# Optimization experiments

Hardware: AMD Instinct MI355X
Metric: run time of the kernel (lower is better)

## Reference

```python
import jax, jax.numpy as jnp
import numpy as np

N = 100000
E = 1600000
D_IN = 128
H = 128


def _param(key, shape, scale=0.05):
    return jax.random.normal(key, shape, dtype=jnp.float32) * scale


def setup_inputs() -> dict:
    key = jax.random.key(0)
    ks = jax.random.split(key, 24)
    inp = {
        'x': jax.random.normal(ks[0], (N, D_IN), dtype=jnp.float32),
        'edge_index': jax.random.randint(ks[1], (2, E), 0, N, dtype=jnp.int64),
        'h1': jax.random.normal(ks[2], (N, H), dtype=jnp.float32),
        'h2': jax.random.normal(ks[3], (N, H), dtype=jnp.float32),
        'h3': jax.random.normal(ks[4], (N, H), dtype=jnp.float32),
        # GCNConv params (PyG: lin weight applied as x @ W, W: [in, out] here)
        'gcn1_w': _param(ks[5], (D_IN, H)),
        'gcn1_b': jnp.zeros((H,), jnp.float32),
        'gcn2_w': _param(ks[6], (H, H)),
        'gcn2_b': jnp.zeros((H,), jnp.float32),
    }
    # torch.nn.GRUCell params: weight_ih [3H, in], weight_hh [3H, H], biases [3H]
    for i, kw in zip((1, 2, 3), (ks[7], ks[10], ks[13])):
        k1, k2, k3 = jax.random.split(kw, 3)
        inp[f'gru{i}_wih'] = _param(k1, (3 * H, H))
        inp[f'gru{i}_whh'] = _param(k2, (3 * H, H))
        inp[f'gru{i}_bih'] = _param(k3, (3 * H,))
        inp[f'gru{i}_bhh'] = jnp.zeros((3 * H,), jnp.float32)
    return inp


def gcn_conv(x, src, dst, w, b):
    """PyG GCNConv: D^-1/2 (A+I) D^-1/2 X W + b (symmetric norm, self-loops)."""
    xw = x @ w  # [N, H]
    ones = jnp.ones((src.shape[0],), xw.dtype)
    # degree including self-loop
    deg = jax.ops.segment_sum(ones, dst, num_segments=N) + 1.0
    dinv = jax.lax.rsqrt(deg)
    norm = dinv[src] * dinv[dst]  # [E]
    agg = jax.ops.segment_sum(xw[src] * norm[:, None], dst, num_segments=N)
    # self-loop contribution: norm = dinv[i]*dinv[i] = 1/deg[i]
    return agg + xw / deg[:, None] + b


def gru_cell(x, h, w_ih, w_hh, b_ih, b_hh):
    gi = x @ w_ih.T + b_ih  # [N, 3H]
    gh = h @ w_hh.T + b_hh
    i_r, i_z, i_n = jnp.split(gi, 3, axis=-1)
    h_r, h_z, h_n = jnp.split(gh, 3, axis=-1)
    r = jax.nn.sigmoid(i_r + h_r)
    z = jax.nn.sigmoid(i_z + h_z)
    n = jnp.tanh(i_n + r * h_n)
    return (1.0 - z) * n + z * h


def reference(x, edge_index, h1, h2, h3,
              gcn1_w, gcn1_b, gcn2_w, gcn2_b,
              gru1_wih, gru1_whh, gru1_bih, gru1_bhh,
              gru2_wih, gru2_whh, gru2_bih, gru2_bhh,
              gru3_wih, gru3_whh, gru3_bih, gru3_bhh):
    src, dst = edge_index[0], edge_index[1]
    x = jax.nn.relu(gcn_conv(x, src, dst, gcn1_w, gcn1_b))
    # dropout is identity at eval
    x = jax.nn.relu(gcn_conv(x, src, dst, gcn2_w, gcn2_b))
    h1n = gru_cell(x, h1, gru1_wih, gru1_whh, gru1_bih, gru1_bhh)
    h2n = gru_cell(h1n, h2, gru2_wih, gru2_whh, gru2_bih, gru2_bhh)
    h3n = gru_cell(h2n, h3, gru3_wih, gru3_whh, gru3_bih, gru3_bhh)
    return (h1n, h2n, h3n)
```

## Files before the change

kernel.cpp:

```cpp
#include <hip/hip_runtime.h>
#include <hip/hip_bf16.h>

#define DH 128
#define SCB 1024
#define NCHUNK 256

typedef __attribute__((ext_vector_type(8))) short short8_t;
typedef __attribute__((ext_vector_type(4))) float f32x4;

static __device__ __forceinline__ short f2bf(float f) {
    union { float f; unsigned u; } v; v.f = f;
    unsigned r = v.u + 0x7fffu + ((v.u >> 16) & 1u);
    return (short)(r >> 16);
}

static __device__ __forceinline__ float bf2f(unsigned short b) {
    union { unsigned u; float f; } v; v.u = ((unsigned)b) << 16;
    return v.f;
}

static __device__ __forceinline__ short8_t cvt8(const float* p) {
    float4 a0 = *(const float4*)p;
    float4 a1 = *(const float4*)(p + 4);
    short8_t t;
    t[0] = f2bf(a0.x); t[1] = f2bf(a0.y); t[2] = f2bf(a0.z); t[3] = f2bf(a0.w);
    t[4] = f2bf(a1.x); t[5] = f2bf(a1.y); t[6] = f2bf(a1.z); t[7] = f2bf(a1.w);
    return t;
}

__global__ __launch_bounds__(256) void deg2_k(const int* __restrict__ ei, int E,
                                              unsigned* __restrict__ cnt, int span, int chunkE) {
    int r = blockIdx.x & 7;
    int c = blockIdx.x >> 3;
    int lo = r * span, hi = lo + span;
    long long e0 = (long long)c * chunkE;
    long long e1 = e0 + chunkE; if (e1 > E) e1 = E;
    for (long long e = e0 + threadIdx.x; e < e1; e += 256) {
        int d = ei[E + e];
        if (d >= lo && d < hi) atomicAdd(&cnt[d], 1u);
    }
}

__global__ __launch_bounds__(256) void scan1_k(const unsigned* __restrict__ cnt, int N,
                                               int* __restrict__ offs, unsigned* __restrict__ bsum) {
    __shared__ unsigned s[256];
    int t = threadIdx.x;
    int i0 = blockIdx.x * SCB + t * 4;
    unsigned v0 = (i0 + 0 < N) ? cnt[i0 + 0] : 0u;
    unsigned v1 = (i0 + 1 < N) ? cnt[i0 + 1] : 0u;
    unsigned v2 = (i0 + 2 < N) ? cnt[i0 + 2] : 0u;
    unsigned v3 = (i0 + 3 < N) ? cnt[i0 + 3] : 0u;
    unsigned ts = v0 + v1 + v2 + v3;
    s[t] = ts;
    __syncthreads();
    for (int off = 1; off < 256; off <<= 1) {
        unsigned u = (t >= off) ? s[t - off] : 0u;
        __syncthreads();
        s[t] += u;
        __syncthreads();
    }
    unsigned ex = s[t] - ts;
    if (i0 + 0 < N) offs[i0 + 0] = (int)ex;
    if (i0 + 1 < N) offs[i0 + 1] = (int)(ex + v0);
    if (i0 + 2 < N) offs[i0 + 2] = (int)(ex + v0 + v1);
    if (i0 + 3 < N) offs[i0 + 3] = (int)(ex + v0 + v1 + v2);
    if (t == 255) bsum[blockIdx.x] = s[255];
}

__global__ __launch_bounds__(1024) void scan2_k(unsigned* __restrict__ bsum, int B) {
    __shared__ unsigned s[1024];
    int t = threadIdx.x;
    unsigned v = (t < B) ? bsum[t] : 0u;
    s[t] = v;
    __syncthreads();
    for (int off = 1; off < 1024; off <<= 1) {
        unsigned u = (t >= off) ? s[t - off] : 0u;
        __syncthreads();
        s[t] += u;
        __syncthreads();
    }
    if (t < B) bsum[t] = s[t] - v;
    if (t == 0) bsum[B] = s[1023];
}

__global__ void scan3_k(int* __restrict__ offs, int* __restrict__ cur,
                        float* __restrict__ dinv, const unsigned* __restrict__ cnt,
                        const unsigned* __restrict__ bsum, int N, int B) {
    int i = blockIdx.x * 256 + threadIdx.x;
    if (i < N) {
        int v = offs[i] + (int)bsum[i >> 10];
        offs[i] = v;
        cur[i] = v;
        dinv[i] = rsqrtf((float)cnt[i] + 1.0f);
    }
    if (i == 0) offs[N] = (int)bsum[B];
}

__global__ __launch_bounds__(256) void fill2_k(const int* __restrict__ ei, int E,
                                               int* __restrict__ cur, int* __restrict__ csr_src,
                                               int span, int chunkE) {
    int r = blockIdx.x & 7;
    int c = blockIdx.x >> 3;
    int lo = r * span, hi = lo + span;
    long long e0 = (long long)c * chunkE;
    long long e1 = e0 + chunkE; if (e1 > E) e1 = E;
    for (long long e = e0 + threadIdx.x; e < e1; e += 256) {
        int d = ei[E + e];
        if (d >= lo && d < hi) {
            int pos = atomicAdd(&cur[d], 1);
            csr_src[pos] = ei[e];
        }
    }
}

__global__ void f2bf6_k(const float* __restrict__ s0, const float* __restrict__ s1,
                        const float* __restrict__ s2, const float* __restrict__ s3,
                        const float* __restrict__ s4, const float* __restrict__ s5,
                        short* __restrict__ dst, int WN) {
    int i = blockIdx.x * 256 + threadIdx.x;
    if (i >= 6 * WN) return;
    int b = i / WN, r = i - b * WN;
    const float* srcs[6] = {s0, s1, s2, s3, s4, s5};
    dst[i] = f2bf(srcs[b][r]);
}

__global__ void transpose_bf2_k(const float* __restrict__ sa, const float* __restrict__ sb,
                                short* __restrict__ da, short* __restrict__ db) {
    int i = blockIdx.x * 256 + threadIdx.x;
    int m = i >> 14;
    int j = i & 16383;
    int c = j >> 7, k = j & 127;
    const float* s = m ? sb : sa;
    short* d = m ? db : da;
    d[j] = f2bf(s[k * DH + c]);
}

__global__ __launch_bounds__(256, 4) void gemm_mfma_k(const float* __restrict__ A,
                                                      const short* __restrict__ Wt,
                                                      const float* __restrict__ dinv,
                                                      short* __restrict__ C, int N) {
    int tid = threadIdx.x;
    int wave = tid >> 6, lane = tid & 63;
    int lr = lane & 15, kg = lane >> 4;

    int row0 = blockIdx.x * 128 + wave * 32;
    int ar0 = min(row0 + lr, N - 1);
    int ar1 = min(row0 + 16 + lr, N - 1);
    const float* a0p = A + (size_t)ar0 * DH;
    const float* a1p = A + (size_t)ar1 * DH;
    short8_t af[2][4];
#pragma unroll
    for (int ks = 0; ks < 4; ks++) {
        af[0][ks] = cvt8(a0p + ks * 32 + kg * 8);
        af[1][ks] = cvt8(a1p + ks * 32 + kg * 8);
    }

    float di0[4], di1[4];
#pragma unroll
    for (int j = 0; j < 4; j++) {
        di0[j] = dinv[min(row0 + kg * 4 + j, N - 1)];
        di1[j] = dinv[min(row0 + 16 + kg * 4 + j, N - 1)];
    }

    short8_t bt[3][4];
#define GLOADW(slot, t) { \
    const short* wp = Wt + (size_t)((t) * 16 + lr) * DH + kg * 8; \
    bt[slot][0] = *(const short8_t*)(wp); \
    bt[slot][1] = *(const short8_t*)(wp + 32); \
    bt[slot][2] = *(const short8_t*)(wp + 64); \
    bt[slot][3] = *(const short8_t*)(wp + 96); }

    GLOADW(0, 0)
    GLOADW(1, 1)
#pragma unroll
    for (int t = 0; t < 8; t++) {
        if (t < 6) GLOADW((t + 2) % 3, t + 2)
        f32x4 acc0 = {0.f, 0.f, 0.f, 0.f};
        f32x4 acc1 = {0.f, 0.f, 0.f, 0.f};
#pragma unroll
        for (int ks = 0; ks < 4; ks++) {
            acc0 = __builtin_amdgcn_mfma_f32_16x16x32_bf16(af[0][ks], bt[t % 3][ks], acc0, 0, 0, 0);
            acc1 = __builtin_amdgcn_mfma_f32_16x16x32_bf16(af[1][ks], bt[t % 3][ks], acc1, 0, 0, 0);
        }
        int col = t * 16 + lr;
#pragma unroll
        for (int j = 0; j < 4; j++) {
            int g0 = row0 + kg * 4 + j;
            int g1 = row0 + 16 + kg * 4 + j;
            if (g0 < N) C[(size_t)g0 * DH + col] = f2bf(acc0[j] * di0[j]);
            if (g1 < N) C[(size_t)g1 * DH + col] = f2bf(acc1[j] * di1[j]);
        }
    }
#undef GLOADW
}

__global__ __launch_bounds__(256) void gather_k(const int* __restrict__ csr_src,
                                                const int* __restrict__ offs,
                                                const float* __restrict__ dinv,
                                                const unsigned* __restrict__ xws,
                                                const float* __restrict__ bias,
                                                float* __restrict__ dest, int N) {
    int wid = blockIdx.x * 4 + (threadIdx.x >> 6);
    if (wid >= N) return;
    int lane = threadIdx.x & 63;
    int j = offs[wid];
    int end = offs[wid + 1];
    float dd = dinv[wid];

    unsigned xv = xws[(size_t)wid * 64 + lane];
    float ax = bf2f((unsigned short)(xv & 0xffffu));
    float ay = bf2f((unsigned short)(xv >> 16));

#define ACC(w) { ax += bf2f((unsigned short)((w) & 0xffffu)); \
                 ay += bf2f((unsigned short)((w) >> 16)); }

    if (j + 4 <= end) {
        int a0 = csr_src[j], a1 = csr_src[j + 1], a2 = csr_src[j + 2], a3 = csr_src[j + 3];
        j += 4;
        for (; j + 4 <= end; j += 4) {
            unsigned w0 = xws[(size_t)a0 * 64 + lane];
            unsigned w1 = xws[(size_t)a1 * 64 + lane];
            unsigned w2 = xws[(size_t)a2 * 64 + lane];
            unsigned w3 = xws[(size_t)a3 * 64 + lane];
            a0 = csr_src[j]; a1 = csr_src[j + 1]; a2 = csr_src[j + 2]; a3 = csr_src[j + 3];
            ACC(w0) ACC(w1) ACC(w2) ACC(w3)
        }
        unsigned w0 = xws[(size_t)a0 * 64 + lane];
        unsigned w1 = xws[(size_t)a1 * 64 + lane];
        unsigned w2 = xws[(size_t)a2 * 64 + lane];
        unsigned w3 = xws[(size_t)a3 * 64 + lane];
        ACC(w0) ACC(w1) ACC(w2) ACC(w3)
    }
    for (; j < end; ++j) {
        unsigned w = xws[(size_t)csr_src[j] * 64 + lane];
        ACC(w)
    }
#undef ACC

    float2 b2 = ((const float2*)bias)[lane];
    float ox = fmaxf(fmaf(dd, ax, b2.x), 0.f);
    float oy = fmaxf(fmaf(dd, ay, b2.y), 0.f);
    float2 o; o.x = ox; o.y = oy;
    ((float2*)dest)[(size_t)wid * 64 + lane] = o;
}

__global__ __launch_bounds__(512, 1) void gru_mfma_k(const float* __restrict__ X,
                                                     const float* __restrict__ Hs,
                                                     const short* __restrict__ wih,
                                                     const short* __restrict__ whh,
                                                     const float* __restrict__ bih,
                                                     const float* __restrict__ bhh,
                                                     float* __restrict__ out, int N) {
    __shared__ short lds[2][64 * DH];
    int tid = threadIdx.x;
    int row0 = blockIdx.x * 64;
    int wave = tid >> 6, lane = tid & 63;
    int lr = lane & 15, kg = lane >> 4;
    int c0 = wave * 16;

    short8_t bw[3][4], bu[3][4];
#pragma unroll
    for (int g = 0; g < 3; g++) {
        const short* wi = wih + (size_t)(g * DH + c0 + lr) * DH + kg * 8;
        const short* wh = whh + (size_t)(g * DH + c0 + lr) * DH + kg * 8;
#pragma unroll
        for (int ks = 0; ks < 4; ks++) {
            bw[g][ks] = *(const short8_t*)(wi + ks * 32);
            bu[g][ks] = *(const short8_t*)(wh + ks * 32);
        }
    }

    {
        int mat = tid >> 8;
        int r = (tid & 255) >> 2;
        int q = tid & 3;
        int grow = min(row0 + r, N - 1);
        const float* src = (mat ? Hs : X) + (size_t)grow * DH + q * 32;
        char* dst = (char*)&lds[mat][r * DH];
#pragma unroll
        for (int j = 0; j < 4; j++) {
            short8_t v = cvt8(src + j * 8);
            int boff = (q * 64 + j * 16) ^ ((r & 7) << 4);
            *(short8_t*)(dst + boff) = v;
        }
    }
    __syncthreads();

    f32x4 aR[4], aZ[4], aI[4], aH[4];
#pragma unroll
    for (int rt = 0; rt < 4; rt++) {
        aR[rt] = (f32x4){0,0,0,0}; aZ[rt] = (f32x4){0,0,0,0};
        aI[rt] = (f32x4){0,0,0,0}; aH[rt] = (f32x4){0,0,0,0};
    }

#pragma unroll
    for (int rt = 0; rt < 4; rt++) {
        int r = rt * 16 + lr;
        char* xrow = (char*)&lds[0][r * DH];
        char* hrow = (char*)&lds[1][r * DH];
        short8_t xa[4], ha[4];
#pragma unroll
        for (int ks = 0; ks < 4; ks++) {
            int boff = (ks * 64 + kg * 16) ^ ((r & 7) << 4);
            xa[ks] = *(short8_t*)(xrow + boff);
            ha[ks] = *(short8_t*)(hrow + boff);
        }
#pragma unroll
        for (int ks = 0; ks < 4; ks++) {
            aR[rt] = __builtin_amdgcn_mfma_f32_16x16x32_bf16(xa[ks], bw[0][ks], aR[rt], 0, 0, 0);
            aR[rt] = __builtin_amdgcn_mfma_f32_16x16x32_bf16(ha[ks], bu[0][ks], aR[rt], 0, 0, 0);
            aZ[rt] = __builtin_amdgcn_mfma_f32_16x16x32_bf16(xa[ks], bw[1][ks], aZ[rt], 0, 0, 0);
            aZ[rt] = __builtin_amdgcn_mfma_f32_16x16x32_bf16(ha[ks], bu[1][ks], aZ[rt], 0, 0, 0);
            aI[rt] = __builtin_amdgcn_mfma_f32_16x16x32_bf16(xa[ks], bw[2][ks], aI[rt], 0, 0, 0);
            aH[rt] = __builtin_amdgcn_mfma_f32_16x16x32_bf16(ha[ks], bu[2][ks], aH[rt], 0, 0, 0);
        }
    }

    int gcol = c0 + lr;
    float br = bih[gcol], bz = bih[DH + gcol], bn = bih[2 * DH + gcol];
    float cr = bhh[gcol], cz = bhh[DH + gcol], cn = bhh[2 * DH + gcol];
#pragma unroll
    for (int rt = 0; rt < 4; rt++) {
#pragma unroll
        for (int j = 0; j < 4; j++) {
            int grow = row0 + rt * 16 + kg * 4 + j;
            if (grow < N) {
                float hv = Hs[(size_t)grow * DH + gcol];
                float r = 1.f / (1.f + __expf(-(aR[rt][j] + br + cr)));
                float z = 1.f / (1.f + __expf(-(aZ[rt][j] + bz + cz)));
                float n = tanhf(aI[rt][j] + bn + r * (aH[rt][j] + cn));
                out[(size_t)grow * DH + gcol] = (1.f - z) * n + z * hv;
            }
        }
    }
}

extern "C" void kernel_launch(void* const* d_in, const int* in_sizes, int n_in,
                              void* d_out, int out_size, void* d_ws, size_t ws_size,
                              hipStream_t stream) {
    const float* x    = (const float*)d_in[0];
    const int*   ei   = (const int*)d_in[1];
    const float* h1   = (const float*)d_in[2];
    const float* h2   = (const float*)d_in[3];
    const float* h3   = (const float*)d_in[4];
    const float* g1w  = (const float*)d_in[5];
    const float* g1b  = (const float*)d_in[6];
    const float* g2w  = (const float*)d_in[7];
    const float* g2b  = (const float*)d_in[8];
    const float* wih1 = (const float*)d_in[9];
    const float* whh1 = (const float*)d_in[10];
    const float* bih1 = (const float*)d_in[11];
    const float* bhh1 = (const float*)d_in[12];
    const float* wih2 = (const float*)d_in[13];
    const float* whh2 = (const float*)d_in[14];
    const float* bih2 = (const float*)d_in[15];
    const float* bhh2 = (const float*)d_in[16];
    const float* wih3 = (const float*)d_in[17];
    const float* whh3 = (const float*)d_in[18];
    const float* bih3 = (const float*)d_in[19];
    const float* bhh3 = (const float*)d_in[20];

    int N = in_sizes[0] / DH;
    int E = in_sizes[1] / 2;
    int B = (N + SCB - 1) / SCB;
    int nstripes = (N + 127) / 128;
    int nblk64 = (N + 63) / 64;
    int span = (N + 7) / 8;
    int chunkE = (E + NCHUNK - 1) / NCHUNK;

    char* wsp = (char*)d_ws;
    auto alloc = [&](size_t bytes) -> char* {
        char* p = wsp;
        wsp += (bytes + 63) & ~(size_t)63;
        return p;
    };
    unsigned* cnt = (unsigned*)alloc((size_t)N * 4);
    int* offs     = (int*)alloc(((size_t)N + 1) * 4);
    int* cur      = (int*)alloc((size_t)N * 4);
    float* dinv   = (float*)alloc((size_t)N * 4);
    unsigned* bsum= (unsigned*)alloc(((size_t)B + 1) * 4);
    int* csr_src  = (int*)alloc((size_t)E * 4);
    short* xwb    = (short*)alloc((size_t)N * DH * 2);
    float* x2     = (float*)alloc((size_t)N * DH * 4);
    short* w1t    = (short*)alloc((size_t)DH * DH * 2);
    short* w2t    = (short*)alloc((size_t)DH * DH * 2);
    const int WN = 3 * DH * DH;
    short* wbAll  = (short*)alloc((size_t)6 * WN * 2);
    short* wb[6];
    for (int i = 0; i < 6; i++) wb[i] = wbAll + (size_t)i * WN;

    float* out  = (float*)d_out;
    float* h1n  = out;
    float* h2n  = out + (size_t)N * DH;
    float* h3n  = out + 2 * (size_t)N * DH;

    f2bf6_k<<<(6 * WN + 255) / 256, 256, 0, stream>>>(wih1, whh1, wih2, whh2, wih3, whh3, wbAll, WN);
    transpose_bf2_k<<<(2 * DH * DH + 255) / 256, 256, 0, stream>>>(g1w, g2w, w1t, w2t);

    hipMemsetAsync(cnt, 0, (size_t)N * 4, stream);
    deg2_k<<<8 * NCHUNK, 256, 0, stream>>>(ei, E, cnt, span, chunkE);
    scan1_k<<<B, 256, 0, stream>>>(cnt, N, offs, bsum);
    scan2_k<<<1, 1024, 0, stream>>>(bsum, B);
    scan3_k<<<(N + 255) / 256, 256, 0, stream>>>(offs, cur, dinv, cnt, bsum, N, B);
    fill2_k<<<8 * NCHUNK, 256, 0, stream>>>(ei, E, cur, csr_src, span, chunkE);

    int gblocks = (N + 3) / 4;

    gemm_mfma_k<<<nstripes, 256, 0, stream>>>(x, w1t, dinv, xwb, N);
    gather_k<<<gblocks, 256, 0, stream>>>(csr_src, offs, dinv, (const unsigned*)xwb, g1b, x2, N);

    gemm_mfma_k<<<nstripes, 256, 0, stream>>>(x2, w2t, dinv, xwb, N);
    gather_k<<<gblocks, 256, 0, stream>>>(csr_src, offs, dinv, (const unsigned*)xwb, g2b, x2, N);

    gru_mfma_k<<<nblk64, 512, 0, stream>>>(x2,  h1, wb[0], wb[1], bih1, bhh1, h1n, N);
    gru_mfma_k<<<nblk64, 512, 0, stream>>>(h1n, h2, wb[2], wb[3], bih2, bhh2, h2n, N);
    gru_mfma_k<<<nblk64, 512, 0, stream>>>(h2n, h3, wb[4], wb[5], bih3, bhh3, h3n, N);
}
```

Baseline: 646.9 us.

## Fuse three GRU cells into one kernel keeping hidden state in LDS

Replaces three separate GRU kernel launches with one kernel that runs all three cells per 64-row tile. Each cell's output is converted to bf16 and written into LDS as the next cell's input, so h1n and h2n are no longer re-read from global memory. The old hidden state is also read from LDS rather than global memory, and sigmoid/tanh now use fast reciprocal-based approximations. The cost is extra barriers and reloading weights into registers between cells, plus slightly lower precision from the bf16 rounding of intermediate outputs and the approximate activations.

```diff
diff --git a/kernel.cpp b/kernel.cpp
--- a/kernel.cpp
+++ b/kernel.cpp
@@ -26,6 +26,13 @@
     t[0] = f2bf(a0.x); t[1] = f2bf(a0.y); t[2] = f2bf(a0.z); t[3] = f2bf(a0.w);
     t[4] = f2bf(a1.x); t[5] = f2bf(a1.y); t[6] = f2bf(a1.z); t[7] = f2bf(a1.w);
     return t;
+}
+
+static __device__ __forceinline__ float sigm(float x) {
+    return __builtin_amdgcn_rcpf(1.f + __expf(-x));
+}
+static __device__ __forceinline__ float tanh_f(float x) {
+    return 1.f - 2.f * __builtin_amdgcn_rcpf(__expf(2.f * x) + 1.f);
 }
 
 __global__ __launch_bounds__(256) void deg2_k(const int* __restrict__ ei, int E,
@@ -244,13 +251,17 @@
     ((float2*)dest)[(size_t)wid * 64 + lane] = o;
 }
 
-__global__ __launch_bounds__(512, 1) void gru_mfma_k(const float* __restrict__ X,
-                                                     const float* __restrict__ Hs,
-                                                     const short* __restrict__ wih,
-                                                     const short* __restrict__ whh,
-                                                     const float* __restrict__ bih,
-                                                     const float* __restrict__ bhh,
-                                                     float* __restrict__ out, int N) {
+__global__ __launch_bounds__(512, 1) void gru3_mfma_k(
+        const float* __restrict__ X, const float* __restrict__ H1,
+        const float* __restrict__ H2, const float* __restrict__ H3,
+        const short* __restrict__ w1i, const short* __restrict__ w1h,
+        const short* __restrict__ w2i, const short* __restrict__ w2h,
+        const short* __restrict__ w3i, const short* __restrict__ w3h,
+        const float* __restrict__ bi1, const float* __restrict__ bh1,
+        const float* __restrict__ bi2, const float* __restrict__ bh2,
+        const float* __restrict__ bi3, const float* __restrict__ bh3,
+        float* __restrict__ o1, float* __restrict__ o2, float* __restrict__ o3,
+        int N) {
     __shared__ short lds[2][64 * DH];
     int tid = threadIdx.x;
     int row0 = blockIdx.x * 64;
@@ -258,24 +269,34 @@
     int lr = lane & 15, kg = lane >> 4;
     int c0 = wave * 16;
 
+    const short* wihs[3] = {w1i, w2i, w3i};
+    const short* whhs[3] = {w1h, w2h, w3h};
+    const float* bihs[3] = {bi1, bi2, bi3};
+    const float* bhhs[3] = {bh1, bh2, bh3};
+    const float* hnexts[2] = {H2, H3};
+    float* outs[3] = {o1, o2, o3};
+
     short8_t bw[3][4], bu[3][4];
-#pragma unroll
-    for (int g = 0; g < 3; g++) {
-        const short* wi = wih + (size_t)(g * DH + c0 + lr) * DH + kg * 8;
-        const short* wh = whh + (size_t)(g * DH + c0 + lr) * DH + kg * 8;
-#pragma unroll
-        for (int ks = 0; ks < 4; ks++) {
-            bw[g][ks] = *(const short8_t*)(wi + ks * 32);
-            bu[g][ks] = *(const short8_t*)(wh + ks * 32);
-        }
-    }
+#define WLOADALL(wih_, whh_) { \
+    _Pragma("unroll") \
+    for (int g = 0; g < 3; g++) { \
+        const short* wi = (wih_) + (size_t)(g * DH + c0 + lr) * DH + kg * 8; \
+        const short* wh = (whh_) + (size_t)(g * DH + c0 + lr) * DH + kg * 8; \
+        _Pragma("unroll") \
+        for (int ks = 0; ks < 4; ks++) { \
+            bw[g][ks] = *(const short8_t*)(wi + ks * 32); \
+            bu[g][ks] = *(const short8_t*)(wh + ks * 32); \
+        } \
+    } }
+
+    WLOADALL(w1i, w1h)
 
     {
         int mat = tid >> 8;
         int r = (tid & 255) >> 2;
         int q = tid & 3;
         int grow = min(row0 + r, N - 1);
-        const float* src = (mat ? Hs : X) + (size_t)grow * DH + q * 32;
+        const float* src = (mat ? H1 : X) + (size_t)grow * DH + q * 32;
         char* dst = (char*)&lds[mat][r * DH];
 #pragma unroll
         for (int j = 0; j < 4; j++) {
@@ -286,53 +307,94 @@
     }
     __syncthreads();
 
-    f32x4 aR[4], aZ[4], aI[4], aH[4];
-#pragma unroll
-    for (int rt = 0; rt < 4; rt++) {
-        aR[rt] = (f32x4){0,0,0,0}; aZ[rt] = (f32x4){0,0,0,0};
-        aI[rt] = (f32x4){0,0,0,0}; aH[rt] = (f32x4){0,0,0,0};
-    }
-
-#pragma unroll
-    for (int rt = 0; rt < 4; rt++) {
-        int r = rt * 16 + lr;
-        char* xrow = (char*)&lds[0][r * DH];
-        char* hrow = (char*)&lds[1][r * DH];
-        short8_t xa[4], ha[4];
-#pragma unroll
-        for (int ks = 0; ks < 4; ks++) {
-            int boff = (ks * 64 + kg * 16) ^ ((r & 7) << 4);
-            xa[ks] = *(short8_t*)(xrow + boff);
-            ha[ks] = *(short8_t*)(hrow + boff);
-        }
-#pragma unroll
-        for (int ks = 0; ks < 4; ks++) {
-            aR[rt] = __builtin_amdgcn_mfma_f32_16x16x32_bf16(xa[ks], bw[0][ks], aR[rt], 0, 0, 0);
-            aR[rt] = __builtin_amdgcn_mfma_f32_16x16x32_bf16(ha[ks], bu[0][ks], aR[rt], 0, 0, 0);
-            aZ[rt] = __builtin_amdgcn_mfma_f32_16x16x32_bf16(xa[ks], bw[1][ks], aZ[rt], 0, 0, 0);
-            aZ[rt] = __builtin_amdgcn_mfma_f32_16x16x32_bf16(ha[ks], bu[1][ks], aZ[rt], 0, 0, 0);
-            aI[rt] = __builtin_amdgcn_mfma_f32_16x16x32_bf16(xa[ks], bw[2][ks], aI[rt], 0, 0, 0);
-            aH[rt] = __builtin_amdgcn_mfma_f32_16x16x32_bf16(ha[ks], bu[2][ks], aH[rt], 0, 0, 0);
-        }
-    }
-
     int gcol = c0 + lr;
-    float br = bih[gcol], bz = bih[DH + gcol], bn = bih[2 * DH + gcol];
-    float cr = bhh[gcol], cz = bhh[DH + gcol], cn = bhh[2 * DH + gcol];
-#pragma unroll
-    for (int rt = 0; rt < 4; rt++) {
-#pragma unroll
-        for (int j = 0; j < 4; j++) {
-            int grow = row0 + rt * 16 + kg * 4 + j;
-            if (grow < N) {
-                float hv = Hs[(size_t)grow * DH + gcol];
-                float r = 1.f / (1.f + __expf(-(aR[rt][j] + br + cr)));
-                float z = 1.f / (1.f + __expf(-(aZ[rt][j] + bz + cz)));
-                float n = tanhf(aI[rt][j] + bn + r * (aH[rt][j] + cn));
-                out[(size_t)grow * DH + gcol] = (1.f - z) * n + z * hv;
+    int colb = gcol * 2;
+
+#pragma unroll
+    for (int cell = 0; cell < 3; cell++) {
+        f32x4 aR[4], aZ[4], aI[4], aH[4];
+#pragma unroll
+        for (int rt = 0; rt < 4; rt++) {
+            aR[rt] = (f32x4){0,0,0,0}; aZ[rt] = (f32x4){0,0,0,0};
+            aI[rt] = (f32x4){0,0,0,0}; aH[rt] = (f32x4){0,0,0,0};
+        }
+#pragma unroll
+        for (int rt = 0; rt < 4; rt++) {
+            int r = rt * 16 + lr;
+            char* xrow = (char*)&lds[0][r * DH];
+            char* hrow = (char*)&lds[1][r * DH];
+            short8_t xa[4], ha[4];
+#pragma unroll
+            for (int ks = 0; ks < 4; ks++) {
+                int boff = (ks * 64 + kg * 16) ^ ((r & 7) << 4);
+                xa[ks] = *(short8_t*)(xrow + boff);
+                ha[ks] = *(short8_t*)(hrow + boff);
             }
-        }
-    }
+#pragma unroll
+            for (int ks = 0; ks < 4; ks++) {
+                aR[rt] = __builtin_amdgcn_mfma_f32_16x16x32_bf16(xa[ks], bw[0][ks], aR[rt], 0, 0, 0);
+                aR[rt] = __builtin_amdgcn_mfma_f32_16x16x32_bf16(ha[ks], bu[0][ks], aR[rt], 0, 0, 0);
+                aZ[rt] = __builtin_amdgcn_mfma_f32_16x16x32_bf16(xa[ks], bw[1][ks], aZ[rt], 0, 0, 0);
+                aZ[rt] = __builtin_amdgcn_mfma_f32_16x16x32_bf16(ha[ks], bu[1][ks], aZ[rt], 0, 0, 0);
+                aI[rt] = __builtin_amdgcn_mfma_f32_16x16x32_bf16(xa[ks], bw[2][ks], aI[rt], 0, 0, 0);
+                aH[rt] = __builtin_amdgcn_mfma_f32_16x16x32_bf16(ha[ks], bu[2][ks], aH[rt], 0, 0, 0);
+            }
+        }
+
+        const float* bih = bihs[cell];
+        const float* bhh = bhhs[cell];
+        float br = bih[gcol], bz = bih[DH + gcol], bn = bih[2 * DH + gcol];
+        float cr = bhh[gcol], cz = bhh[DH + gcol], cn = bhh[2 * DH + gcol];
+        float* outp = outs[cell];
+        short hb[4][4];
+#pragma unroll
+        for (int rt = 0; rt < 4; rt++) {
+#pragma unroll
+            for (int j = 0; j < 4; j++) {
+                int r = rt * 16 + kg * 4 + j;
+                float hv = bf2f(*(unsigned short*)((char*)&lds[1][r * DH] + (colb ^ ((r & 7) << 4))));
+                float rr = sigm(aR[rt][j] + br + cr);
+                float zz = sigm(aZ[rt][j] + bz + cz);
+                float nn = tanh_f(aI[rt][j] + bn + rr * (aH[rt][j] + cn));
+                float ov = (1.f - zz) * nn + zz * hv;
+                int grow = row0 + r;
+                if (grow < N) outp[(size_t)grow * DH + gcol] = ov;
+                hb[rt][j] = f2bf(ov);
+            }
+        }
+
+        if (cell < 2) {
+            WLOADALL(wihs[cell + 1], whhs[cell + 1])
+        }
+
+        __syncthreads();
+
+        if (cell < 2) {
+#pragma unroll
+            for (int rt = 0; rt < 4; rt++) {
+#pragma unroll
+                for (int j = 0; j < 4; j++) {
+                    int r = rt * 16 + kg * 4 + j;
+                    *(short*)((char*)&lds[0][r * DH] + (colb ^ ((r & 7) << 4))) = hb[rt][j];
+                }
+            }
+            {
+                int r = tid >> 3;
+                int q = tid & 7;
+                int grow = min(row0 + r, N - 1);
+                const float* src = hnexts[cell] + (size_t)grow * DH + q * 16;
+                char* dst = (char*)&lds[1][r * DH];
+#pragma unroll
+                for (int j = 0; j < 2; j++) {
+                    short8_t v = cvt8(src + j * 8);
+                    int boff = (q * 32 + j * 16) ^ ((r & 7) << 4);
+                    *(short8_t*)(dst + boff) = v;
+                }
+            }
+            __syncthreads();
+        }
+    }
+#undef WLOADALL
 }
 
 extern "C" void kernel_launch(void* const* d_in, const int* in_sizes, int n_in,
@@ -412,7 +474,8 @@
     gemm_mfma_k<<<nstripes, 256, 0, stream>>>(x2, w2t, dinv, xwb, N);
     gather_k<<<gblocks, 256, 0, stream>>>(csr_src, offs, dinv, (const unsigned*)xwb, g2b, x2, N);
 
-    gru_mfma_k<<<nblk64, 512, 0, stream>>>(x2,  h1, wb[0], wb[1], bih1, bhh1, h1n, N);
-    gru_mfma_k<<<nblk64, 512, 0, stream>>>(h1n, h2, wb[2], wb[3], bih2, bhh2, h2n, N);
-    gru_mfma_k<<<nblk64, 512, 0, stream>>>(h2n, h3, wb[4], wb[5], bih3, bhh3, h3n, N);
-}
+    gru3_mfma_k<<<nblk64, 512, 0, stream>>>(x2, h1, h2, h3,
+                                            wb[0], wb[1], wb[2], wb[3], wb[4], wb[5],
+                                            bih1, bhh1, bih2, bhh2, bih3, bhh3,
+                                            h1n, h2n, h3n, N);
+}
```

Measured after the change: 575.5 us. -11.0%, faster.
